# Optimization experiments

Hardware: AMD Instinct MI355X
Metric: run time of the kernel (lower is better)

## Reference

```python
import jax, jax.numpy as jnp
import numpy as np

B, C, H, W = 4, 128, 128, 128
NCLS = 80
NCONV = 2


def conv3x3(x, w, b):
    # x: [B,Cin,H,W], w: [Cout,Cin,3,3]
    y = jax.lax.conv_general_dilated(x, w, (1, 1), 'SAME',
                                     dimension_numbers=('NCHW', 'OIHW', 'NCHW'))
    return y + b[None, :, None, None]


def setup_inputs() -> dict:
    key = jax.random.key(0)
    ks = jax.random.split(key, 10)
    std = 0.01  # conv init std in the torch module
    prior_prob = 0.01
    bias_value = -np.log((1 - prior_prob) / prior_prob)
    inp = {
        'feature': jax.random.normal(ks[0], (B, C, H, W), jnp.float32),
        'targets': jax.random.uniform(ks[1], (B, NCLS, H, W), jnp.float32),
        'cls_w': std * jax.random.normal(ks[2], (NCONV, C, C, 3, 3), jnp.float32),
        'cls_b': jnp.zeros((NCONV, C), jnp.float32),
        'bbox_w': std * jax.random.normal(ks[3], (NCONV, C, C, 3, 3), jnp.float32),
        'bbox_b': jnp.zeros((NCONV, C), jnp.float32),
        'off_w': std * jax.random.normal(ks[4], (NCONV, C, C, 3, 3), jnp.float32),
        'off_b': jnp.zeros((NCONV, C), jnp.float32),
        'cls_score_w': std * jax.random.normal(ks[5], (NCLS, C, 3, 3), jnp.float32),
        'cls_score_b': jnp.full((NCLS,), bias_value, jnp.float32),
        'bbox_pred_w': std * jax.random.normal(ks[6], (2, C, 3, 3), jnp.float32),
        'bbox_pred_b': jnp.zeros((2,), jnp.float32),
        'center_off_w': std * jax.random.normal(ks[7], (2, C, 3, 3), jnp.float32),
        'center_off_b': jnp.zeros((2,), jnp.float32),
        'K': 100,
    }
    return inp


def centernet_forward(feature, targets, cls_w, cls_b, bbox_w, bbox_b, off_w, off_b,
                      cls_score_w, cls_score_b, bbox_pred_w, bbox_pred_b,
                      center_off_w, center_off_b, K):
    # ---- head: three conv+ReLU subnets + final 3x3 heads ----
    xc, xb, xo = feature, feature, feature
    for i in range(NCONV):
        xc = jax.nn.relu(conv3x3(xc, cls_w[i], cls_b[i]))
        xb = jax.nn.relu(conv3x3(xb, bbox_w[i], bbox_b[i]))
        xo = jax.nn.relu(conv3x3(xo, off_w[i], off_b[i]))
    logits = conv3x3(xc, cls_score_w, cls_score_b)      # [B,NCLS,H,W]
    wh = conv3x3(xb, bbox_pred_w, bbox_pred_b)          # [B,2,H,W]
    off = conv3x3(xo, center_off_w, center_off_b)       # [B,2,H,W]

    # ---- center focal loss (alpha=2, beta=4, reduction='sum') ----
    pos = (targets == 1.0).astype(logits.dtype)
    neg = (targets < 1.0).astype(logits.dtype)
    neg_w = jnp.power(1.0 - targets, 4.0)
    p = jax.nn.sigmoid(logits)
    log_p = jax.nn.log_sigmoid(logits)        # log(sigmoid(x))
    log_1mp = jax.nn.log_sigmoid(-logits)     # log(1 - sigmoid(x))
    pos_loss = log_p * jnp.square(1.0 - p) * pos
    neg_loss = log_1mp * jnp.square(p) * neg_w * neg
    loss = -(pos_loss.sum()) - (neg_loss.sum())

    # ---- decode: sigmoid + 3x3 maxpool pseudo-NMS + top-k + gather ----
    hm = p  # sigmoid heatmap
    hmax = jax.lax.reduce_window(hm, -jnp.inf, jax.lax.max,
                                 (1, 1, 3, 3), (1, 1, 1, 1), 'SAME')
    hm_nms = jnp.where(hmax == hm, hm, 0.0)
    scores, inds = jax.lax.top_k(hm_nms.reshape(B, -1), K)  # [B,K]
    hw = H * W
    clses = inds // hw                 # [B,K] int class ids
    sp = inds % hw                     # spatial index
    ys = (sp // W).astype(jnp.float32)
    xs = (sp % W).astype(jnp.float32)
    # gather wh/offset at peak locations
    wh_k = jnp.take_along_axis(wh.reshape(B, 2, hw), sp[:, None, :], axis=2)    # [B,2,K]
    off_k = jnp.take_along_axis(off.reshape(B, 2, hw), sp[:, None, :], axis=2)  # [B,2,K]
    cx = xs + off_k[:, 0]
    cy = ys + off_k[:, 1]
    w_, h_ = wh_k[:, 0], wh_k[:, 1]
    boxes = jnp.stack([cx - w_ / 2, cy - h_ / 2, cx + w_ / 2, cy + h_ / 2], axis=-1)  # [B,K,4]
    return boxes, scores, clses, loss


def reference(feature, targets, cls_w, cls_b, bbox_w, bbox_b, off_w, off_b,
              cls_score_w, cls_score_b, bbox_pred_w, bbox_pred_b,
              center_off_w, center_off_b, K):
    return centernet_forward(feature, targets, cls_w, cls_b, bbox_w, bbox_b,
                             off_w, off_b, cls_score_w, cls_score_b,
                             bbox_pred_w, bbox_pred_b, center_off_w,
                             center_off_b, K)
```

## Files before the change

kernel.cpp:

```cpp
#include <hip/hip_runtime.h>
#include <hip/hip_bf16.h>
#include <math.h>

#define B_    4
#define C_    128
#define H_    128
#define W_    128
#define HW_   (H_*W_)
#define NCLS_ 80
#define KTOP  100
#define CAPB  2048

typedef __attribute__((ext_vector_type(8)))  short bf16x8;
typedef __attribute__((ext_vector_type(16))) float f32x16;

#define WSTG_B     16384
#define WIMG_B     589824
#define NIMG       7
#define XROWB      144
#define XCOLS      130
#define XPITCH     (XCOLS * XROWB)
#define XSZ        ((size_t)16 * 130 * XPITCH)
#define XLDS_B     25920
#define LDS_TOT    (2 * XLDS_B)
#define ZERO_N     20512

__device__ __forceinline__ unsigned bf16_rne(float x) {
    unsigned u = __float_as_uint(x);
    return (u + 0x7FFFu + ((u >> 16) & 1u)) >> 16;
}
__device__ __forceinline__ void split2(float v0, float v1, unsigned& hiP, unsigned& loP) {
    unsigned h0 = bf16_rne(v0), h1 = bf16_rne(v1);
    float r0 = v0 - __uint_as_float(h0 << 16);
    float r1 = v1 - __uint_as_float(h1 << 16);
    unsigned l0 = bf16_rne(r0), l1 = bf16_rne(r1);
    hiP = h0 | (h1 << 16);
    loP = l0 | (l1 << 16);
}

#define MFMA32(a, bvec, c) __builtin_amdgcn_mfma_f32_32x32x16_bf16(a, bvec, c, 0, 0, 0)

__global__ __launch_bounds__(256) void init_k(char* __restrict__ xbase, int nbuf,
                                              unsigned* __restrict__ sm, float* __restrict__ loss)
{
    const int i = blockIdx.x * 256 + threadIdx.x;
    const int nb = nbuf * 8256;
    if (i < nb) {
        char* buf = xbase + (size_t)(i / 8256) * XSZ;
        const int j = i % 8256;
        int R, col;
        if (j < 4160) {
            const int g = j / 260, rr = j % 260;
            R = g * 130 + ((rr < 130) ? 0 : 129);
            col = rr % 130;
        } else {
            const int q = j - 4160;
            const int g = q / 256, m = q % 256;
            R = g * 130 + 1 + (m >> 1);
            col = (m & 1) ? 129 : 0;
        }
        char* p = buf + ((size_t)R * XCOLS + col) * XROWB;
        #pragma unroll
        for (int k = 0; k < 9; k++) *(uint4*)(p + k * 16) = make_uint4(0, 0, 0, 0);
    } else {
        const int k = i - nb;
        if (k < ZERO_N) sm[k] = 0u;
        if (k == ZERO_N) *loss = 0.f;
    }
}

struct WtArgs { const float* src[NIMG]; int cout[NIMG]; };

__global__ __launch_bounds__(256) void wtx_k(WtArgs a, unsigned short* wt)
{
    const int img = blockIdx.z;
    const int idx = blockIdx.x * 256 + threadIdx.x;
    const int h  = idx & 1;
    const int ks = (idx >> 1) & 1;
    const int r  = (idx >> 2) & 31;
    const int g  = (idx >> 7) & 3;
    const int st = idx >> 9;
    if (st >= 36) return;
    const int tap = st % 9, chunk = st / 9;
    const float* w = a.src[img];
    const int Cout = a.cout[img];
    const int cout = g * 32 + r;
    const int cin0 = chunk * 32 + ks * 16 + h * 8;
    float v[8];
    #pragma unroll
    for (int j = 0; j < 8; j++)
        v[j] = (cout < Cout) ? w[((size_t)cout * 128 + cin0 + j) * 9 + tap] : 0.f;
    unsigned hiW[4], loW[4];
    #pragma unroll
    for (int j = 0; j < 4; j++) split2(v[2 * j], v[2 * j + 1], hiW[j], loW[j]);
    char* dst = (char*)wt + (size_t)img * WIMG_B + (size_t)st * WSTG_B
              + g * 4096 + ks * 2048 + r * 32 + h * 16;
    *(uint4*)dst          = make_uint4(hiW[0], hiW[1], hiW[2], hiW[3]);
    *(uint4*)(dst + 1024) = make_uint4(loW[0], loW[1], loW[2], loW[3]);
}

template<int RELU, int XOUT>
__device__ __forceinline__ void conv_epilogue(
    f32x16 (&acc)[2][2], const bool* act,
    const float* bias, float* outf, char* outx, int Cout,
    int b, int x0, int y0, int wm, int wn, int kh, int l31)
{
    #pragma unroll
    for (int f = 0; f < 2; f++) {
        if (!act[f]) continue;
        if (XOUT == 0) {
            #pragma unroll
            for (int r = 0; r < 16; r++) {
                const int co = wm * 64 + f * 32 + 4 * kh + (r & 3) + 8 * (r >> 2);
                if (co < Cout) {
                    const float bv = bias[co];
                    #pragma unroll
                    for (int fn = 0; fn < 2; fn++) {
                        const int p = wn * 64 + fn * 32 + l31;
                        float v = acc[f][fn][r] + bv;
                        if (RELU) v = fmaxf(v, 0.f);
                        outf[((size_t)b * Cout + co) * HW_ + (size_t)(y0 + (p >> 4)) * 128 + (x0 + (p & 15))] = v;
                    }
                }
// ... 106 lines not shown
            if ((unsigned)gy < 128u && (unsigned)gx < 128u) {                 \
                const float* p0 = inb + (size_t)((ch) * 32 + 2 * cp) * HW_    \
                                      + gy * 128 + gx;                        \
                v0 = p0[0]; v1 = p0[HW_];                                     \
            }                                                                 \
        }                                                                     \
        xa[it] = v0; xb[it] = v1;                                             \
    }                                                                         \
} while (0)

#define STOREX_F(bufsel) do {                                                 \
    _Pragma("unroll")                                                         \
    for (int it = 0; it < 12; it++) {                                         \
        const int idx = t + it * 256;                                         \
        const int pl = idx & 15, cp = (idx >> 4) & 15, ph = idx >> 8;         \
        const int pos = ph * 16 + pl;                                         \
        if (pos < 180) {                                                      \
            unsigned hiP, loP; split2(xa[it], xb[it], hiP, loP);              \
            *(unsigned*)(lds + (bufsel) * XLDS_B + pos * 144 + 4 * cp)      = hiP; \
            *(unsigned*)(lds + (bufsel) * XLDS_B + pos * 144 + 64 + 4 * cp) = loP; \
        }                                                                     \
    }                                                                         \
} while (0)

#define TAPF_(CH, TAP, CUR, NXT) do {                                         \
    if ((CH) * 9 + (TAP) + 1 < 36) WLOAD_(NXT, (CH) * 9 + (TAP) + 1);         \
    MFMA_TAP_(CUR, (((TAP) / 3) * 18 + ((TAP) % 3)) * 144 + ((CH) & 1) * XLDS_B); \
} while (0)

#define CHUNKF_(CH, SA, SB) do {                                              \
    TAPF_(CH, 0, SA, SB); TAPF_(CH, 1, SB, SA); TAPF_(CH, 2, SA, SB);         \
    TAPF_(CH, 3, SB, SA); TAPF_(CH, 4, SA, SB); TAPF_(CH, 5, SB, SA);         \
    if ((CH) < 3) LOADX_F((CH) + 1);                                          \
    TAPF_(CH, 6, SA, SB); TAPF_(CH, 7, SB, SA); TAPF_(CH, 8, SA, SB);         \
    if ((CH) < 3) { STOREX_F(((CH) + 1) & 1); __syncthreads(); }              \
} while (0)

#define CONVF_MAIN()                                                          \
    bf16x8 wf[2][8];                                                          \
    WLOAD_(0, 0);                                                             \
    float xa[12], xb[12];                                                     \
    LOADX_F(0);                                                               \
    STOREX_F(0);                                                              \
    __syncthreads();                                                          \
    CHUNKF_(0, 0, 1);                                                         \
    CHUNKF_(1, 1, 0);                                                         \
    CHUNKF_(2, 0, 1);                                                         \
    CHUNKF_(3, 1, 0);

template<int RELU, int XOUT>
__global__ __launch_bounds__(256, 2) void conv_f_k(
    const float* __restrict__ in, const unsigned short* __restrict__ wt,
    const float* __restrict__ bias, float* __restrict__ outf,
    char* __restrict__ outx, int Cout)
{
    CONVF_SETUP();
    bool act[2];
    #pragma unroll
    for (int f = 0; f < 2; f++) act[f] = (wm * 64 + f * 32) < Cout;
    const char* wb = (const char*)wt + wm * 8192 + wlane;
    const float* inb = in + (size_t)b * 128 * HW_;
    CONVF_MAIN();
    conv_epilogue<RELU, XOUT>(acc, act, bias, outf, outx, Cout, b, x0, y0, wm, wn, kh, l31);
}

struct F3Args { const unsigned short* wt[3]; const float* bias[3]; char* outx[3]; };

__global__ __launch_bounds__(256, 2) void convF3_k(const float* __restrict__ in, F3Args a)
{
    const int ty = blockIdx.y;
    const unsigned short* wt = a.wt[ty];
    const float* bias = a.bias[ty];
    char* outx = a.outx[ty];

    CONVF_SETUP();
    bool act[2]; act[0] = true; act[1] = true;
    const char* wb = (const char*)wt + wm * 8192 + wlane;
    const float* inb = in + (size_t)b * 128 * HW_;
    CONVF_MAIN();
    conv_epilogue<1, 1>(acc, act, bias, nullptr, outx, 128, b, x0, y0, wm, wn, kh, l31);
}

#define CONVX_SETUP()                                                         \
    __shared__ __align__(16) char lds[LDS_TOT];                               \
    const int t    = threadIdx.x;                                             \
    const int lane = t & 63;                                                  \
    const int wv   = t >> 6;                                                  \
    const int wm   = wv >> 1;                                                 \
    const int wn   = wv & 1;                                                  \
    const int l31  = lane & 31;                                               \
    const int kh   = lane >> 5;                                               \
    const int bi = blockIdx.x;                                                \
    const int x0 = (bi & 7) << 4;                                             \
    const int y0 = ((bi >> 3) & 15) << 3;                                     \
    const int b  = bi >> 7;                                                   \
    int baddr[2];                                                             \
    _Pragma("unroll")                                                         \
    for (int fn = 0; fn < 2; fn++) {                                          \
        const int p = wn * 64 + fn * 32 + l31;                                \
        baddr[fn] = (p >> 4) * 2592 + (p & 15) * 144 + kh * 16;               \
    }                                                                         \
    const int wlane = ((lane & 31) << 5) | (kh << 4);                         \
    f32x16 acc[2][2];                                                         \
    _Pragma("unroll")                                                         \
    for (int i_ = 0; i_ < 2; i_++)                                            \
        _Pragma("unroll")                                                     \
        for (int j_ = 0; j_ < 2; j_++)                                        \
            _Pragma("unroll")                                                 \
            for (int r_ = 0; r_ < 16; r_++) acc[i_][j_][r_] = 0.f;

#define CONVX_PROLOG()                                                        \
    {                                                                         \
        const size_t rowbase = ((size_t)((b * 4 + 0) * 130 + y0) * XCOLS + x0) * XROWB; \
        _Pragma("unroll")                                                     \
        for (int gg = 0; gg < 5; gg++) {                                      \
            const int g = wv * 5 + gg;                                        \
            const int hy = g >> 1, i = g & 1;                                 \
            __builtin_amdgcn_global_load_lds(                                 \
                (const __attribute__((address_space(1))) unsigned*)           \
                    (xin + rowbase + (size_t)hy * XPITCH + i * 1024 + lane * 16), \
                (__attribute__((address_space(3))) unsigned*)(lds + hy * 2592 + i * 1024), \
                16, 0, 0);                                                    \
        }                                                                     \
        for (int u = t; u < 340; u += 256) {                                  \
            const int hy = u / 34;                                            \
            const int off = 2048 + (u % 34) * 16;                             \
            uint4 v = *(const uint4*)(xin + rowbase + (size_t)hy * XPITCH + off); \
            *(uint4*)(lds + hy * 2592 + off) = v;                             \
        }                                                                     \
    }                                                                         \
    __syncthreads();

#define TAPX_(CH, TAP, CUR, NXT) do {                                         \
    if ((CH) * 9 + (TAP) + 1 < 36) WLOAD_(NXT, (CH) * 9 + (TAP) + 1);         \
    MFMA_TAP_(CUR, ((TAP) / 3) * 2592 + ((TAP) % 3) * 144 + ((CH) & 1) * XLDS_B); \
} while (0)

#define CHUNKX_(CH, SA, SB) do {                                              \
    uint4 tl0_, tl1_; bool h1_ = false;                                       \
    const int xd_ = (((CH) + 1) & 1) * XLDS_B;                                \
    if ((CH) < 3) {                                                           \
        const size_t rowb1_ = ((size_t)((b * 4 + (CH) + 1) * 130 + y0) * XCOLS + x0) * XROWB; \
        _Pragma("unroll")                                                     \
        for (int gg = 0; gg < 5; gg++) {                                      \
            const int g = wv * 5 + gg;                                        \
            const int hy = g >> 1, ii = g & 1;                                \
            __builtin_amdgcn_global_load_lds(                                 \
                (const __attribute__((address_space(1))) unsigned*)           \
                    (xin + rowb1_ + (size_t)hy * XPITCH + ii * 1024 + lane * 16), \
                (__attribute__((address_space(3))) unsigned*)(lds + xd_ + hy * 2592 + ii * 1024), \
                16, 0, 0);                                                    \
        }                                                                     \
        {                                                                     \
            const int hy = t / 34, off = 2048 + (t % 34) * 16;                \
            tl0_ = *(const uint4*)(xin + rowb1_ + (size_t)hy * XPITCH + off); \
        }                                                                     \
        h1_ = (t < 84);                                                       \
        if (h1_) {                                                            \
            const int u = t + 256;                                            \
            const int hy = u / 34, off = 2048 + (u % 34) * 16;                \
            tl1_ = *(const uint4*)(xin + rowb1_ + (size_t)hy * XPITCH + off); \
        }                                                                     \
    }                                                                         \
    TAPX_(CH, 0, SA, SB); TAPX_(CH, 1, SB, SA); TAPX_(CH, 2, SA, SB);         \
    TAPX_(CH, 3, SB, SA); TAPX_(CH, 4, SA, SB); TAPX_(CH, 5, SB, SA);         \
    TAPX_(CH, 6, SA, SB); TAPX_(CH, 7, SB, SA); TAPX_(CH, 8, SA, SB);         \
    if ((CH) < 3) {                                                           \
        {                                                                     \
            const int hy = t / 34, off = 2048 + (t % 34) * 16;                \
            *(uint4*)(lds + xd_ + hy * 2592 + off) = tl0_;                    \
        }                                                                     \
        if (h1_) {                                                            \
            const int u = t + 256;                                            \
            const int hy = u / 34, off = 2048 + (u % 34) * 16;                \
            *(uint4*)(lds + xd_ + hy * 2592 + off) = tl1_;                    \
        }                                                                     \
        __syncthreads();                                                      \
    }                                                                         \
} while (0)

#define CONVX_MAIN()                                                          \
    bf16x8 wf[2][8];                                                          \
    WLOAD_(0, 0);                                                             \
    CONVX_PROLOG();                                                           \
    CHUNKX_(0, 0, 1);                                                         \
    CHUNKX_(1, 1, 0);                                                         \
    CHUNKX_(2, 0, 1);                                                         \
    CHUNKX_(3, 1, 0);

template<int RELU, int XOUT>
__global__ __launch_bounds__(256, 2) void conv_x_k(
    const char* __restrict__ xin, const unsigned short* __restrict__ wt,
    const float* __restrict__ bias, float* __restrict__ outf,
    char* __restrict__ outx, int Cout)
{
    CONVX_SETUP();
    bool act[2];
    #pragma unroll
    for (int f = 0; f < 2; f++) act[f] = (wm * 64 + f * 32) < Cout;
    const char* wb = (const char*)wt + wm * 8192 + wlane;
    CONVX_MAIN();
    conv_epilogue<RELU, XOUT>(acc, act, bias, outf, outx, Cout, b, x0, y0, wm, wn, kh, l31);
}

struct X3Args {
    const char* xin[3]; const unsigned short* wt[3]; const float* bias[3];
    float* outf[3]; char* outx[3]; int xout[3];
};

__global__ __launch_bounds__(256, 2) void convX3_k(X3Args a)
{
    const int ty = blockIdx.y;
    const char* xin = a.xin[ty];
    const unsigned short* wt = a.wt[ty];
    const float* bias = a.bias[ty];
    float* outf = a.outf[ty];
    char* outx = a.outx[ty];
    const int xo = a.xout[ty];

    CONVX_SETUP();
    bool act[2]; act[0] = true; act[1] = true;
    const char* wb = (const char*)wt + wm * 8192 + wlane;
    CONVX_MAIN();
    if (xo) conv_epilogue<1, 1>(acc, act, bias, nullptr, outx, 128, b, x0, y0, wm, wn, kh, l31);
    else    conv_epilogue<1, 0>(acc, act, bias, outf, nullptr, 128, b, x0, y0, wm, wn, kh, l31);
}

__device__ __forceinline__ void conv2out_body(
    const float* in, const float* w, const float* bias, float* out)
{
    __shared__ float ws[128 * 9 * 2];
    const int t = threadIdx.x;
    for (int i = t; i < 2304; i += 256) {
        const int co = i & 1, tap = (i >> 1) % 9, ci = i / 18;
        ws[i] = w[(size_t)co * 1152 + ci * 9 + tap];
    }
    __syncthreads();

    const int b  = blockIdx.y;
    const int y  = (blockIdx.x >> 3) * 16 + (t >> 4);
    const int x  = (blockIdx.x & 7) * 16 + (t & 15);
    const float* inb = in + (size_t)b * 128 * HW_ + y * 128 + x;

    float a0 = bias[0], a1 = bias[1];
    #pragma unroll 2
    for (int ci = 0; ci < 128; ci++) {
        const float* p  = inb + (size_t)ci * HW_;
        const float* wp = ws + ci * 18;
        #pragma unroll
        for (int tap = 0; tap < 9; tap++) {
            const int dy = tap / 3 - 1, dx = tap % 3 - 1;
            const int yy = y + dy, xx = x + dx;
            float v = 0.f;
            if ((unsigned)yy < 128u && (unsigned)xx < 128u) v = p[dy * 128 + dx];
            a0 = fmaf(v, wp[tap * 2 + 0], a0);
            a1 = fmaf(v, wp[tap * 2 + 1], a1);
        }
    }
    out[((size_t)b * 2 + 0) * HW_ + y * 128 + x] = a0;
    out[((size_t)b * 2 + 1) * HW_ + y * 128 + x] = a1;
}

__global__ __launch_bounds__(256) void conv2out_k(
    const float* __restrict__ in, const float* __restrict__ w,
    const float* __restrict__ bias, float* __restrict__ out)
{
    conv2out_body(in, w, bias, out);
}

__global__ __launch_bounds__(256) void conv2out2_k(
    const float* in0, const float* in1,
    const float* w0, const float* w1,
    const float* b0, const float* b1,
    float* out0, float* out1)
{
    const int z = blockIdx.z;
    conv2out_body(z ? in1 : in0, z ? w1 : w0, z ? b1 : b0, z ? out1 : out0);
}

__global__ __launch_bounds__(256) void lnh_k(
    const float* __restrict__ L, const float* __restrict__ targets,
    float* __restrict__ loss_out, unsigned* __restrict__ keys,
    unsigned* __restrict__ hist)
{
    __shared__ unsigned h[2048];
    for (int j = threadIdx.x; j < 2048; j += 256) h[j] = 0;
    __syncthreads();

    const int per_b = NCLS_ * HW_;
    const int b = blockIdx.y;
    const float* Lb = L + (size_t)b * per_b;
    const float* Tb = targets + (size_t)b * per_b;
    unsigned* kb = keys + (size_t)b * per_b;

    float sum = 0.f;
    for (int i = blockIdx.x * 256 + threadIdx.x; i < per_b; i += gridDim.x * 256) {
        const float x = Lb[i];
        const float t = Tb[i];
        const float e   = expf(-fabsf(x));
        const float inv = 1.f / (1.f + e);
        const float lp  = log1pf(e);
        const bool  xe  = (x >= 0.f);
        const float p   = xe ? inv : e * inv;
        const float lsp = xe ? -lp : (x - lp);
        const float lsn = lsp - x;
        float om = 1.f - t;
        float nw = om * om; nw *= nw;
        const float omp = 1.f - p;
        if (t == 1.0f)     sum -= lsp * omp * omp;
        else if (t < 1.0f) sum -= lsn * p * p * nw;

        const int sp = i & (HW_ - 1);
        const int y = sp >> 7, xq = sp & 127;
        const float* plane = Lb + (i - sp);
        const int ym = (y > 0) ? y - 1 : 0,   yp = (y < 127) ? y + 1 : 127;
        const int xm = (xq > 0) ? xq - 1 : 0, xp = (xq < 127) ? xq + 1 : 127;
        const float* r0 = plane + ym * 128;
        const float* r1 = plane + y  * 128;
        const float* r2 = plane + yp * 128;
        float m = fmaxf(fmaxf(fmaxf(r0[xm], r0[xq]), fmaxf(r0[xp], r1[xm])),
                 fmaxf(fmaxf(x, r1[xp]),
                 fmaxf(fmaxf(r2[xm], r2[xq]), r2[xp])));
        const float em   = expf(-fabsf(m));
        const float invm = 1.f / (1.f + em);
        const float pm   = (m >= 0.f) ? invm : em * invm;
        const unsigned key = (__float_as_uint(p) == __float_as_uint(pm)) ? __float_as_uint(p) : 0u;
        kb[i] = key;
        if (key) atomicAdd(&h[key >> 21], 1u);
    }

    #pragma unroll
    for (int off = 32; off > 0; off >>= 1) sum += __shfl_down(sum, off, 64);
    __shared__ float wsum[4];
    int lane = threadIdx.x & 63, wid = threadIdx.x >> 6;
    if (lane == 0) wsum[wid] = sum;
    __syncthreads();
    if (threadIdx.x == 0)
        atomicAdd(loss_out, wsum[0] + wsum[1] + wsum[2] + wsum[3]);

    unsigned* gh = hist + b * 2048;
    for (int j = threadIdx.x; j < 2048; j += 256) if (h[j]) atomicAdd(&gh[j], h[j]);
}

__global__ void hist2_k(const unsigned* __restrict__ keys, const unsigned* __restrict__ bin1,
                        unsigned* __restrict__ hist)
{
    __shared__ unsigned h[2048];
    for (int j = threadIdx.x; j < 2048; j += blockDim.x) h[j] = 0;
    __syncthreads();
    const int per_b = NCLS_ * HW_;
    const int b = blockIdx.y;
    const unsigned b1 = bin1[b];
    const unsigned* kb = keys + (size_t)b * per_b;
    for (int i = blockIdx.x * blockDim.x + threadIdx.x; i < per_b; i += gridDim.x * blockDim.x) {
        unsigned k = kb[i];
        if (k && (k >> 21) == b1) atomicAdd(&h[(k >> 10) & 2047], 1u);
    }
    __syncthreads();
    unsigned* gh = hist + b * 2048;
    for (int j = threadIdx.x; j < 2048; j += blockDim.x) if (h[j]) atomicAdd(&gh[j], h[j]);
}

__global__ void hist3_k(const unsigned* __restrict__ keys, const unsigned* __restrict__ pfx2,
                        unsigned* __restrict__ hist)
{
    __shared__ unsigned h[1024];
    for (int j = threadIdx.x; j < 1024; j += blockDim.x) h[j] = 0;
    __syncthreads();
    const int per_b = NCLS_ * HW_;
    const int b = blockIdx.y;
    const unsigned p2 = pfx2[b];
    const unsigned* kb = keys + (size_t)b * per_b;
    for (int i = blockIdx.x * blockDim.x + threadIdx.x; i < per_b; i += gridDim.x * blockDim.x) {
        unsigned k = kb[i];
        if (k && (k >> 10) == p2) atomicAdd(&h[k & 1023], 1u);
    }
    __syncthreads();
    unsigned* gh = hist + b * 1024;
    for (int j = threadIdx.x; j < 1024; j += blockDim.x) if (h[j]) atomicAdd(&gh[j], h[j]);
}

template<int NBINS, int LEVEL>
__global__ __launch_bounds__(256) void scan_k(
    const unsigned* __restrict__ hist,
    const unsigned* __restrict__ inPfx, const unsigned* __restrict__ inGt,
    unsigned* __restrict__ outPfx, unsigned* __restrict__ outGt)
{
    constexpr int PER = NBINS / 256;
    const int b = blockIdx.x;
    const int t = threadIdx.x;
    const unsigned* h = hist + b * NBINS;
    const unsigned base = (LEVEL == 1) ? 0u : inGt[b];

    unsigned v[PER];
    unsigned local = 0;
    #pragma unroll
    for (int i = 0; i < PER; i++) { v[i] = h[t * PER + i]; local += v[i]; }

    __shared__ unsigned ps[256];
    ps[t] = local;
    __syncthreads();
    #pragma unroll
    for (int off = 1; off < 256; off <<= 1) {
        unsigned add = (t + off < 256) ? ps[t + off] : 0u;
        __syncthreads();
        ps[t] += add;
        __syncthreads();
    }
    const unsigned sumAbove = (t == 255) ? 0u : ps[t + 1];

    unsigned sfx = sumAbove;
    #pragma unroll
    for (int i = PER - 1; i >= 0; i--) {
        unsigned sfx_next = sfx;
        sfx += v[i];
        bool cond     = (base + sfx      >= KTOP);
        bool condNext = (base + sfx_next >= KTOP);
        if (cond && !condNext) {
            unsigned sel = (unsigned)(t * PER + i);
            unsigned pfx = (LEVEL == 1) ? sel
                         : (LEVEL == 2) ? ((inPfx[b] << 11) | sel)
                                        : ((inPfx[b] << 10) | sel);
            outPfx[b] = pfx;
            outGt[b]  = base + sfx_next;
        }
    }
    if (t == 0 && base + ps[0] < KTOP) {
        unsigned pfx = (LEVEL == 1) ? 0u
                     : (LEVEL == 2) ? (inPfx[b] << 11)
                                    : (inPfx[b] << 10);
        outPfx[b] = pfx;
        outGt[b]  = base + ps[0];
    }
}

__global__ void select_k(const unsigned* __restrict__ keys, const unsigned* __restrict__ Tk,
                         unsigned* cntA, unsigned* cntB,
                         uint2* __restrict__ listA, unsigned* __restrict__ listB)
{
    const int per_b = NCLS_ * HW_;
    const int b = blockIdx.y;
    const unsigned T = Tk[b];
    const unsigned* kb = keys + (size_t)b * per_b;
    for (int i = blockIdx.x * blockDim.x + threadIdx.x; i < per_b; i += gridDim.x * blockDim.x) {
        unsigned k = kb[i];
        if (k > T) {
            unsigned pos = atomicAdd(&cntA[b], 1u);
            if (pos < KTOP) listA[b * KTOP + pos] = make_uint2(k, (unsigned)i);
        } else if (k == T && k != 0u) {
            unsigned pos = atomicAdd(&cntB[b], 1u);
            if (pos < CAPB) listB[b * CAPB + pos] = (unsigned)i;
        }
    }
}

__global__ void finalize_k(const unsigned* __restrict__ cntA, const unsigned* __restrict__ cntB,
                           const uint2* __restrict__ listA, const unsigned* __restrict__ listB,
                           const unsigned* __restrict__ Tk,
                           const float* __restrict__ wh, const float* __restrict__ off,
                           float* __restrict__ out)
{
    __shared__ unsigned sk[KTOP], si[KTOP], ok[KTOP], oi[KTOP];
    const int b = blockIdx.x;
    const int nA = (int)min(cntA[b], (unsigned)KTOP);
    const unsigned T = Tk[b];

    if ((int)threadIdx.x < nA) {
        uint2 e = listA[b * KTOP + threadIdx.x];
        sk[threadIdx.x] = e.x;
        si[threadIdx.x] = e.y;
    }
    __syncthreads();

    if (threadIdx.x == 0) {
        int need = KTOP - nA;
        unsigned nB = min(cntB[b], (unsigned)CAPB);
        long long prev = -1;
        for (int r = 0; r < need; r++) {
            unsigned best = 0xFFFFFFFFu;
            for (unsigned j = 0; j < nB; j++) {
                unsigned idx = listB[b * CAPB + j];
                if ((long long)idx > prev && idx < best) best = idx;
            }
            if (best == 0xFFFFFFFFu) { sk[nA + r] = 0u; si[nA + r] = 0u; }
            else { sk[nA + r] = T; si[nA + r] = best; prev = (long long)best; }
        }
    }
    __syncthreads();

    if (threadIdx.x < KTOP) {
        unsigned kk = sk[threadIdx.x], ii = si[threadIdx.x];
        int rank = 0;
        for (int j = 0; j < KTOP; j++) {
            unsigned kj = sk[j], ij = si[j];
            rank += (kj > kk) || (kj == kk && ij < ii);
        }
        ok[rank] = kk; oi[rank] = ii;
    }
    __syncthreads();

    if (threadIdx.x < KTOP) {
        int r = threadIdx.x;
        unsigned ind = oi[r];
        float score = __uint_as_float(ok[r]);
        int cls = (int)(ind / HW_);
        int sp  = (int)(ind % HW_);
        float ysf = (float)(sp >> 7);
        float xsf = (float)(sp & 127);
        float w0 = wh[((size_t)b * 2 + 0) * HW_ + sp];
        float h0 = wh[((size_t)b * 2 + 1) * HW_ + sp];
        float o0 = off[((size_t)b * 2 + 0) * HW_ + sp];
        float o1 = off[((size_t)b * 2 + 1) * HW_ + sp];
        float cx = xsf + o0;
        float cy = ysf + o1;
        float* boxes  = out;
        float* scores = out + (size_t)B_ * KTOP * 4;
        float* clses  = out + (size_t)B_ * KTOP * 5;
        boxes[((size_t)b * KTOP + r) * 4 + 0] = cx - w0 * 0.5f;
        boxes[((size_t)b * KTOP + r) * 4 + 1] = cy - h0 * 0.5f;
        boxes[((size_t)b * KTOP + r) * 4 + 2] = cx + w0 * 0.5f;
        boxes[((size_t)b * KTOP + r) * 4 + 3] = cy + h0 * 0.5f;
        scores[b * KTOP + r] = score;
        clses[b * KTOP + r]  = (float)cls;
    }
}

extern "C" void kernel_launch(void* const* d_in, const int* in_sizes, int n_in,
                              void* d_out, int out_size, void* d_ws, size_t ws_size,
                              hipStream_t stream)
{
    const float* feature      = (const float*)d_in[0];
    const float* targets      = (const float*)d_in[1];
    const float* cls_w        = (const float*)d_in[2];
    const float* cls_b        = (const float*)d_in[3];
    const float* bbox_w       = (const float*)d_in[4];
    const float* bbox_b       = (const float*)d_in[5];
    const float* off_w        = (const float*)d_in[6];
    const float* off_b        = (const float*)d_in[7];
    const float* cls_score_w  = (const float*)d_in[8];
    const float* cls_score_b  = (const float*)d_in[9];
    const float* bbox_pred_w  = (const float*)d_in[10];
    const float* bbox_pred_b  = (const float*)d_in[11];
    const float* center_off_w = (const float*)d_in[12];
    const float* center_off_b = (const float*)d_in[13];
    float* out = (float*)d_out;

    const size_t L_BYTES  = (size_t)B_ * NCLS_ * HW_ * 4;
    const size_t P_BYTES  = (size_t)B_ * 2 * HW_ * 4;
    const size_t WT_BYTES = (size_t)NIMG * WIMG_B;
    const size_t SM_BYTES = (size_t)1 << 18;

    char* ws = (char*)d_ws;
    const size_t lw = (size_t)C_ * C_ * 9;
    float* loss_ptr = out + (size_t)B_ * KTOP * 6;

    WtArgs wa;
    wa.src[0] = cls_w;        wa.cout[0] = 128;
    wa.src[1] = bbox_w;       wa.cout[1] = 128;
    wa.src[2] = off_w;        wa.cout[2] = 128;
    wa.src[3] = cls_w + lw;   wa.cout[3] = 128;
    wa.src[4] = bbox_w + lw;  wa.cout[4] = 128;
    wa.src[5] = off_w + lw;   wa.cout[5] = 128;
    wa.src[6] = cls_score_w;  wa.cout[6] = NCLS_;

    const size_t FUSED_NEED = 6 * XSZ + 2 * P_BYTES + WT_BYTES + SM_BYTES;

    #define WIMG(i) (WT + (size_t)(i) * (WIMG_B / 2))

    if (ws_size >= FUSED_NEED) {
        char* XA0 = ws;
        char* XA1 = ws + XSZ;
        char* XA2 = ws + 2 * XSZ;
        char* XB  = ws + 3 * XSZ;
        float* Bfb = (float*)(ws + 4 * XSZ);
        float* Bfo = (float*)(ws + 5 * XSZ);
        float* L   = (float*)XA0;
        unsigned* keys = (unsigned*)XA1;
        float* WH  = (float*)(ws + 6 * XSZ);
        float* OFF = (float*)(ws + 6 * XSZ + P_BYTES);
        unsigned short* WT = (unsigned short*)(ws + 6 * XSZ + 2 * P_BYTES);
        unsigned* sm = (unsigned*)(ws + 6 * XSZ + 2 * P_BYTES + WT_BYTES);

        unsigned* hist1 = sm;
        unsigned* hist2 = sm + 4 * 2048;
        unsigned* hist3 = sm + 8 * 2048;
        unsigned* bin1  = sm + 8 * 2048 + 4 * 1024;
        unsigned* gt1   = bin1 + 4;
        unsigned* pfx2  = bin1 + 8;
        unsigned* gt2   = bin1 + 12;
        unsigned* Tk    = bin1 + 16;
        unsigned* gt3   = bin1 + 20;
        unsigned* cntA  = bin1 + 24;
        unsigned* cntB  = bin1 + 28;
        uint2*    listA = (uint2*)(bin1 + 32);
        unsigned* listB = (unsigned*)(bin1 + 32 + 2 * B_ * KTOP);

        init_k<<<210, 256, 0, stream>>>(XA0, 4, sm, loss_ptr);
        wtx_k<<<dim3(72, 1, NIMG), 256, 0, stream>>>(wa, WT);

        F3Args f3;
        f3.wt[0] = WIMG(0); f3.bias[0] = cls_b;  f3.outx[0] = XA0;
        f3.wt[1] = WIMG(1); f3.bias[1] = bbox_b; f3.outx[1] = XA1;
        f3.wt[2] = WIMG(2); f3.bias[2] = off_b;  f3.outx[2] = XA2;
        convF3_k<<<dim3(512, 3), 256, 0, stream>>>(feature, f3);

        X3Args x3;
        x3.xin[0] = XA0; x3.wt[0] = WIMG(3); x3.bias[0] = cls_b + C_;
        x3.outf[0] = nullptr; x3.outx[0] = XB; x3.xout[0] = 1;
        x3.xin[1] = XA1; x3.wt[1] = WIMG(4); x3.bias[1] = bbox_b + C_;
        x3.outf[1] = Bfb; x3.outx[1] = nullptr; x3.xout[1] = 0;
        x3.xin[2] = XA2; x3.wt[2] = WIMG(5); x3.bias[2] = off_b + C_;
        x3.outf[2] = Bfo; x3.outx[2] = nullptr; x3.xout[2] = 0;
        convX3_k<<<dim3(512, 3), 256, 0, stream>>>(x3);

        conv_x_k<0, 0><<<512, 256, 0, stream>>>(XB, WIMG(6), cls_score_b, L, nullptr, NCLS_);
        conv2out2_k<<<dim3(64, 4, 2), 256, 0, stream>>>(
            Bfb, Bfo, bbox_pred_w, center_off_w, bbox_pred_b, center_off_b, WH, OFF);

        lnh_k<<<dim3(512, B_), 256, 0, stream>>>(L, targets, loss_ptr, keys, hist1);

        dim3 hgrid(512, B_);
        scan_k<2048, 1><<<B_, 256, 0, stream>>>(hist1, nullptr, nullptr, bin1, gt1);
        hist2_k<<<hgrid, 256, 0, stream>>>(keys, bin1, hist2);
        scan_k<2048, 2><<<B_, 256, 0, stream>>>(hist2, bin1, gt1, pfx2, gt2);
        hist3_k<<<hgrid, 256, 0, stream>>>(keys, pfx2, hist3);
        scan_k<1024, 3><<<B_, 256, 0, stream>>>(hist3, pfx2, gt2, Tk, gt3);
        select_k<<<hgrid, 256, 0, stream>>>(keys, Tk, cntA, cntB, listA, listB);

        finalize_k<<<B_, 128, 0, stream>>>(cntA, cntB, listA, listB, Tk, WH, OFF, out);
    } else {
        char* XA = ws;
        char* XB = ws + XSZ;
        float* L   = (float*)(ws + 2 * XSZ);
        float* WH  = (float*)(ws + 2 * XSZ + L_BYTES);
        float* OFF = (float*)(ws + 2 * XSZ + L_BYTES + P_BYTES);
        unsigned short* WT = (unsigned short*)(ws + 2 * XSZ + L_BYTES + 2 * P_BYTES);
        unsigned* sm = (unsigned*)(ws + 2 * XSZ + L_BYTES + 2 * P_BYTES + WT_BYTES);
        float* Bf = (float*)XB;
        unsigned* keys = (unsigned*)XB;

        unsigned* hist1 = sm;
        unsigned* hist2 = sm + 4 * 2048;
        unsigned* hist3 = sm + 8 * 2048;
        unsigned* bin1  = sm + 8 * 2048 + 4 * 1024;
        unsigned* gt1   = bin1 + 4;
        unsigned* pfx2  = bin1 + 8;
        unsigned* gt2   = bin1 + 12;
        unsigned* Tk    = bin1 + 16;
        unsigned* gt3   = bin1 + 20;
        unsigned* cntA  = bin1 + 24;
        unsigned* cntB  = bin1 + 28;
        uint2*    listA = (uint2*)(bin1 + 32);
        unsigned* listB = (unsigned*)(bin1 + 32 + 2 * B_ * KTOP);

        init_k<<<145, 256, 0, stream>>>(XA, 2, sm, loss_ptr);
        wtx_k<<<dim3(72, 1, NIMG), 256, 0, stream>>>(wa, WT);

        conv_f_k<1, 1><<<512, 256, 0, stream>>>(feature, WIMG(0), cls_b,       nullptr, XA, 128);
        conv_x_k<1, 1><<<512, 256, 0, stream>>>(XA,      WIMG(3), cls_b + C_,  nullptr, XB, 128);
        conv_x_k<0, 0><<<512, 256, 0, stream>>>(XB,      WIMG(6), cls_score_b, L, nullptr, NCLS_);
        conv_f_k<1, 1><<<512, 256, 0, stream>>>(feature, WIMG(1), bbox_b,      nullptr, XA, 128);
        conv_x_k<1, 0><<<512, 256, 0, stream>>>(XA,      WIMG(4), bbox_b + C_, Bf, nullptr, 128);
        conv2out_k<<<dim3(64, 4), 256, 0, stream>>>(Bf, bbox_pred_w, bbox_pred_b, WH);
        conv_f_k<1, 1><<<512, 256, 0, stream>>>(feature, WIMG(2), off_b,       nullptr, XA, 128);
        conv_x_k<1, 0><<<512, 256, 0, stream>>>(XA,      WIMG(5), off_b + C_,  Bf, nullptr, 128);
        conv2out_k<<<dim3(64, 4), 256, 0, stream>>>(Bf, center_off_w, center_off_b, OFF);

        lnh_k<<<dim3(512, B_), 256, 0, stream>>>(L, targets, loss_ptr, keys, hist1);

        dim3 hgrid(512, B_);
        scan_k<2048, 1><<<B_, 256, 0, stream>>>(hist1, nullptr, nullptr, bin1, gt1);
        hist2_k<<<hgrid, 256, 0, stream>>>(keys, bin1, hist2);
        scan_k<2048, 2><<<B_, 256, 0, stream>>>(hist2, bin1, gt1, pfx2, gt2);
        hist3_k<<<hgrid, 256, 0, stream>>>(keys, pfx2, hist3);
        scan_k<1024, 3><<<B_, 256, 0, stream>>>(hist3, pfx2, gt2, Tk, gt3);
        select_k<<<hgrid, 256, 0, stream>>>(keys, Tk, cntA, cntB, listA, listB);

        finalize_k<<<B_, 128, 0, stream>>>(cntA, cntB, listA, listB, Tk, WH, OFF, out);
    }
}
```

Baseline: 548.1 us.

## Fold scan/finalize into last-block of histogram kernels and merge score conv with heads

The separate scan kernels and the finalize kernel are folded into the preceding histogram and select kernels using a last-block-done atomic counter, so the last block to finish runs the scan or finalize. The class-score conv and the two small 2-channel head convs are merged into a single launch with a blockIdx split. The aim is to cut kernel launches and inter-kernel gaps on the serial top-k chain. In exchange, the last block does serial work on a single CU, and the cross-block handoff depends on atomics and fences.

```diff
diff --git a/kernel.cpp b/kernel.cpp
--- a/kernel.cpp
+++ b/kernel.cpp
@@ -23,7 +23,7 @@
 #define XSZ        ((size_t)16 * 130 * XPITCH)
 #define XLDS_B     25920
 #define LDS_TOT    (2 * XLDS_B)
-#define ZERO_N     20512
+#define ZERO_N     20516
 
 __device__ __forceinline__ unsigned bf16_rne(float x) {
     unsigned u = __float_as_uint(x);
@@ -39,6 +39,15 @@
 }
 
 #define MFMA32(a, bvec, c) __builtin_amdgcn_mfma_f32_32x32x16_bf16(a, bvec, c, 0, 0, 0)
+
+__device__ __forceinline__ bool last_block(unsigned* done) {
+    __threadfence();
+    __syncthreads();
+    __shared__ unsigned lb_rank_;
+    if (threadIdx.x == 0) lb_rank_ = atomicAdd(done, 1u);
+    __syncthreads();
+    return lb_rank_ == gridDim.x * gridDim.y - 1;
+}
 
 __global__ __launch_bounds__(256) void init_k(char* __restrict__ xbase, int nbuf,
                                               unsigned* __restrict__ sm, float* __restrict__ loss)
@@ -311,7 +320,6 @@
 }
 
 #define CONVX_SETUP()                                                         \
-    __shared__ __align__(16) char lds[LDS_TOT];                               \
     const int t    = threadIdx.x;                                             \
     const int lane = t & 63;                                                  \
     const int wv   = t >> 6;                                                  \
@@ -423,6 +431,7 @@
     const float* __restrict__ bias, float* __restrict__ outf,
     char* __restrict__ outx, int Cout)
 {
+    __shared__ __align__(16) char lds[LDS_TOT];
     CONVX_SETUP();
     bool act[2];
     #pragma unroll
@@ -439,6 +448,7 @@
 
 __global__ __launch_bounds__(256, 2) void convX3_k(X3Args a)
 {
+    __shared__ __align__(16) char lds[LDS_TOT];
     const int ty = blockIdx.y;
     const char* xin = a.xin[ty];
     const unsigned short* wt = a.wt[ty];
@@ -456,9 +466,9 @@
 }
 
 __device__ __forceinline__ void conv2out_body(
-    const float* in, const float* w, const float* bias, float* out)
-{
-    __shared__ float ws[128 * 9 * 2];
+    const float* in, const float* w, const float* bias, float* out,
+    int gx, int b, float* ws)
+{
     const int t = threadIdx.x;
     for (int i = t; i < 2304; i += 256) {
         const int co = i & 1, tap = (i >> 1) % 9, ci = i / 18;
@@ -466,9 +476,8 @@
     }
     __syncthreads();
 
-    const int b  = blockIdx.y;
-    const int y  = (blockIdx.x >> 3) * 16 + (t >> 4);
-    const int x  = (blockIdx.x & 7) * 16 + (t & 15);
+    const int y  = (gx >> 3) * 16 + (t >> 4);
+    const int x  = (gx & 7) * 16 + (t & 15);
     const float* inb = in + (size_t)b * 128 * HW_ + y * 128 + x;
 
     float a0 = bias[0], a1 = bias[1];
@@ -494,23 +503,100 @@
     const float* __restrict__ in, const float* __restrict__ w,
     const float* __restrict__ bias, float* __restrict__ out)
 {
-    conv2out_body(in, w, bias, out);
-}
-
-__global__ __launch_bounds__(256) void conv2out2_k(
-    const float* in0, const float* in1,
-    const float* w0, const float* w1,
-    const float* b0, const float* b1,
-    float* out0, float* out1)
-{
-    const int z = blockIdx.z;
-    conv2out_body(z ? in1 : in0, z ? w1 : w0, z ? b1 : b0, z ? out1 : out0);
+    __shared__ float ws[2304];
+    conv2out_body(in, w, bias, out, blockIdx.x, blockIdx.y, ws);
+}
+
+__global__ __launch_bounds__(256, 2) void sc_k(
+    const char* __restrict__ xbin, const unsigned short* __restrict__ wt,
+    const float* __restrict__ sbias, float* __restrict__ Lout,
+    const float* __restrict__ inb0, const float* __restrict__ inb1,
+    const float* __restrict__ w0, const float* __restrict__ w1,
+    const float* __restrict__ hb0, const float* __restrict__ hb1,
+    float* __restrict__ WH, float* __restrict__ OFF)
+{
+    __shared__ __align__(16) char lds[LDS_TOT];
+    if (blockIdx.x < 512) {
+        const char* xin = xbin;
+        CONVX_SETUP();
+        bool act[2];
+        act[0] = true; act[1] = (64 < NCLS_);
+        const char* wb = (const char*)wt + wm * 8192 + wlane;
+        CONVX_MAIN();
+        conv_epilogue<0, 0>(acc, act, sbias, Lout, nullptr, NCLS_, b, x0, y0, wm, wn, kh, l31);
+    } else {
+        const int j = blockIdx.x - 512;
+        const int gx = j & 63, bb = (j >> 6) & 3, z = j >> 8;
+        conv2out_body(z ? inb1 : inb0, z ? w1 : w0, z ? hb1 : hb0, z ? OFF : WH,
+                      gx, bb, (float*)lds);
+    }
+}
+
+template<int NBINS, int LEVEL>
+__device__ __forceinline__ void scan_body(
+    unsigned* h, const unsigned* inPfx, const unsigned* inGt,
+    unsigned* outPfx, unsigned* outGt, int b)
+{
+    constexpr int PER = NBINS / 256;
+    const int t = threadIdx.x;
+    const unsigned base = (LEVEL == 1) ? 0u : inGt[b];
+
+    unsigned v[PER];
+    unsigned local = 0;
+    #pragma unroll
+    for (int i = 0; i < PER; i++) { v[i] = atomicAdd(&h[t * PER + i], 0u); local += v[i]; }
+
+    __shared__ unsigned ps[256];
+    ps[t] = local;
+    __syncthreads();
+    #pragma unroll
+    for (int off = 1; off < 256; off <<= 1) {
+        unsigned add = (t + off < 256) ? ps[t + off] : 0u;
+        __syncthreads();
+        ps[t] += add;
+        __syncthreads();
+    }
+    const unsigned sumAbove = (t == 255) ? 0u : ps[t + 1];
+
+    unsigned sfx = sumAbove;
+    #pragma unroll
+    for (int i = PER - 1; i >= 0; i--) {
+        unsigned sfx_next = sfx;
+        sfx += v[i];
+        bool cond     = (base + sfx      >= KTOP);
+        bool condNext = (base + sfx_next >= KTOP);
+        if (cond && !condNext) {
+            unsigned sel = (unsigned)(t * PER + i);
+            unsigned pfx = (LEVEL == 1) ? sel
+                         : (LEVEL == 2) ? ((inPfx[b] << 11) | sel)
+                                        : ((inPfx[b] << 10) | sel);
+            outPfx[b] = pfx;
+            outGt[b]  = base + sfx_next;
+        }
+    }
+    if (t == 0 && base + ps[0] < KTOP) {
+        unsigned pfx = (LEVEL == 1) ? 0u
+                     : (LEVEL == 2) ? (inPfx[b] << 11)
+                                    : (inPfx[b] << 10);
+        outPfx[b] = pfx;
+        outGt[b]  = base + ps[0];
+    }
+}
+
+template<int NBINS, int LEVEL>
+__global__ __launch_bounds__(256) void scan_k(
+    unsigned* __restrict__ hist,
+    const unsigned* __restrict__ inPfx, const unsigned* __restrict__ inGt,
+    unsigned* __restrict__ outPfx, unsigned* __restrict__ outGt)
+{
+    scan_body<NBINS, LEVEL>(hist + blockIdx.x * NBINS, inPfx, inGt, outPfx, outGt, blockIdx.x);
 }
 
 __global__ __launch_bounds__(256) void lnh_k(
     const float* __restrict__ L, const float* __restrict__ targets,
     float* __restrict__ loss_out, unsigned* __restrict__ keys,
-    unsigned* __restrict__ hist)
+    unsigned* __restrict__ hist,
+    unsigned* done, unsigned* outPfx, unsigned* outGt)
 {
     __shared__ unsigned h[2048];
     for (int j = threadIdx.x; j < 2048; j += 256) h[j] = 0;
@@ -569,10 +655,19 @@
 
     unsigned* gh = hist + b * 2048;
     for (int j = threadIdx.x; j < 2048; j += 256) if (h[j]) atomicAdd(&gh[j], h[j]);
-}
-
-__global__ void hist2_k(const unsigned* __restrict__ keys, const unsigned* __restrict__ bin1,
-                        unsigned* __restrict__ hist)
+
+    if (done && last_block(done)) {
+        for (int bb = 0; bb < B_; bb++) {
+            scan_body<2048, 1>(hist + bb * 2048, nullptr, nullptr, outPfx, outGt, bb);
+            __syncthreads();
+        }
+    }
+}
+
+__global__ __launch_bounds__(256) void hist2_k(
+    const unsigned* __restrict__ keys, const unsigned* __restrict__ bin1,
+    unsigned* __restrict__ hist,
+    unsigned* done, const unsigned* inGt, unsigned* outPfx, unsigned* outGt)
 {
     __shared__ unsigned h[2048];
     for (int j = threadIdx.x; j < 2048; j += blockDim.x) h[j] = 0;
@@ -588,10 +683,19 @@
     __syncthreads();
     unsigned* gh = hist + b * 2048;
     for (int j = threadIdx.x; j < 2048; j += blockDim.x) if (h[j]) atomicAdd(&gh[j], h[j]);
-}
-
-__global__ void hist3_k(const unsigned* __restrict__ keys, const unsigned* __restrict__ pfx2,
-                        unsigned* __restrict__ hist)
+
+    if (done && last_block(done)) {
+        for (int bb = 0; bb < B_; bb++) {
+            scan_body<2048, 2>(hist + bb * 2048, bin1, inGt, outPfx, outGt, bb);
+            __syncthreads();
+        }
+    }
+}
+
+__global__ __launch_bounds__(256) void hist3_k(
+    const unsigned* __restrict__ keys, const unsigned* __restrict__ pfx2,
+    unsigned* __restrict__ hist,
+    unsigned* done, const unsigned* inGt, unsigned* outPfx, unsigned* outGt)
 {
     __shared__ unsigned h[1024];
     for (int j = threadIdx.x; j < 1024; j += blockDim.x) h[j] = 0;
@@ -607,108 +711,42 @@
     __syncthreads();
     unsigned* gh = hist + b * 1024;
     for (int j = threadIdx.x; j < 1024; j += blockDim.x) if (h[j]) atomicAdd(&gh[j], h[j]);
-}
-
-template<int NBINS, int LEVEL>
-__global__ __launch_bounds__(256) void scan_k(
-    const unsigned* __restrict__ hist,
-    const unsigned* __restrict__ inPfx, const unsigned* __restrict__ inGt,
-    unsigned* __restrict__ outPfx, unsigned* __restrict__ outGt)
-{
-    constexpr int PER = NBINS / 256;
-    const int b = blockIdx.x;
+
+    if (done && last_block(done)) {
+        for (int bb = 0; bb < B_; bb++) {
+            scan_body<1024, 3>(hist + bb * 1024, pfx2, inGt, outPfx, outGt, bb);
+            __syncthreads();
+        }
+    }
+}
+
+__device__ __forceinline__ void finalize_body(
+    unsigned long long* listA, unsigned* listB,
+    const unsigned* Tk, unsigned* cntA, unsigned* cntB,
+    const float* wh, const float* off, float* out, int b)
+{
+    __shared__ unsigned sk[KTOP], si[KTOP], ok[KTOP], oi[KTOP];
+    __shared__ unsigned lbs[CAPB];
     const int t = threadIdx.x;
-    const unsigned* h = hist + b * NBINS;
-    const unsigned base = (LEVEL == 1) ? 0u : inGt[b];
-
-    unsigned v[PER];
-    unsigned local = 0;
-    #pragma unroll
-    for (int i = 0; i < PER; i++) { v[i] = h[t * PER + i]; local += v[i]; }
-
-    __shared__ unsigned ps[256];
-    ps[t] = local;
-    __syncthreads();
-    #pragma unroll
-    for (int off = 1; off < 256; off <<= 1) {
-        unsigned add = (t + off < 256) ? ps[t + off] : 0u;
-        __syncthreads();
-        ps[t] += add;
-        __syncthreads();
-    }
-    const unsigned sumAbove = (t == 255) ? 0u : ps[t + 1];
-
-    unsigned sfx = sumAbove;
-    #pragma unroll
-    for (int i = PER - 1; i >= 0; i--) {
-        unsigned sfx_next = sfx;
-        sfx += v[i];
-        bool cond     = (base + sfx      >= KTOP);
-        bool condNext = (base + sfx_next >= KTOP);
-        if (cond && !condNext) {
-            unsigned sel = (unsigned)(t * PER + i);
-            unsigned pfx = (LEVEL == 1) ? sel
-                         : (LEVEL == 2) ? ((inPfx[b] << 11) | sel)
-                                        : ((inPfx[b] << 10) | sel);
-            outPfx[b] = pfx;
-            outGt[b]  = base + sfx_next;
-        }
-    }
-    if (t == 0 && base + ps[0] < KTOP) {
-        unsigned pfx = (LEVEL == 1) ? 0u
-                     : (LEVEL == 2) ? (inPfx[b] << 11)
-                                    : (inPfx[b] << 10);
-        outPfx[b] = pfx;
-        outGt[b]  = base + ps[0];
-    }
-}
-
-__global__ void select_k(const unsigned* __restrict__ keys, const unsigned* __restrict__ Tk,
-                         unsigned* cntA, unsigned* cntB,
-                         uint2* __restrict__ listA, unsigned* __restrict__ listB)
-{
-    const int per_b = NCLS_ * HW_;
-    const int b = blockIdx.y;
+    const int nA = (int)min(atomicAdd(&cntA[b], 0u), (unsigned)KTOP);
+    const unsigned nB = min(atomicAdd(&cntB[b], 0u), (unsigned)CAPB);
     const unsigned T = Tk[b];
-    const unsigned* kb = keys + (size_t)b * per_b;
-    for (int i = blockIdx.x * blockDim.x + threadIdx.x; i < per_b; i += gridDim.x * blockDim.x) {
-        unsigned k = kb[i];
-        if (k > T) {
-            unsigned pos = atomicAdd(&cntA[b], 1u);
-            if (pos < KTOP) listA[b * KTOP + pos] = make_uint2(k, (unsigned)i);
-        } else if (k == T && k != 0u) {
-            unsigned pos = atomicAdd(&cntB[b], 1u);
-            if (pos < CAPB) listB[b * CAPB + pos] = (unsigned)i;
-        }
-    }
-}
-
-__global__ void finalize_k(const unsigned* __restrict__ cntA, const unsigned* __restrict__ cntB,
-                           const uint2* __restrict__ listA, const unsigned* __restrict__ listB,
-                           const unsigned* __restrict__ Tk,
-                           const float* __restrict__ wh, const float* __restrict__ off,
-                           float* __restrict__ out)
-{
-    __shared__ unsigned sk[KTOP], si[KTOP], ok[KTOP], oi[KTOP];
-    const int b = blockIdx.x;
-    const int nA = (int)min(cntA[b], (unsigned)KTOP);
-    const unsigned T = Tk[b];
-
-    if ((int)threadIdx.x < nA) {
-        uint2 e = listA[b * KTOP + threadIdx.x];
-        sk[threadIdx.x] = e.x;
-        si[threadIdx.x] = e.y;
-    }
-    __syncthreads();
-
-    if (threadIdx.x == 0) {
+
+    if (t < nA) {
+        unsigned long long v = atomicAdd(&listA[b * KTOP + t], 0ull);
+        sk[t] = (unsigned)v;
+        si[t] = (unsigned)(v >> 32);
+    }
+    for (int j = t; j < (int)nB; j += 256) lbs[j] = atomicAdd(&listB[b * CAPB + j], 0u);
+    __syncthreads();
+
+    if (t == 0) {
         int need = KTOP - nA;
-        unsigned nB = min(cntB[b], (unsigned)CAPB);
         long long prev = -1;
         for (int r = 0; r < need; r++) {
             unsigned best = 0xFFFFFFFFu;
             for (unsigned j = 0; j < nB; j++) {
-                unsigned idx = listB[b * CAPB + j];
+                unsigned idx = lbs[j];
                 if ((long long)idx > prev && idx < best) best = idx;
             }
             if (best == 0xFFFFFFFFu) { sk[nA + r] = 0u; si[nA + r] = 0u; }
@@ -717,8 +755,8 @@
     }
     __syncthreads();
 
-    if (threadIdx.x < KTOP) {
-        unsigned kk = sk[threadIdx.x], ii = si[threadIdx.x];
+    if (t < KTOP) {
+        unsigned kk = sk[t], ii = si[t];
         int rank = 0;
         for (int j = 0; j < KTOP; j++) {
             unsigned kj = sk[j], ij = si[j];
@@ -728,8 +766,8 @@
     }
     __syncthreads();
 
-    if (threadIdx.x < KTOP) {
-        int r = threadIdx.x;
+    if (t < KTOP) {
+        int r = t;
         unsigned ind = oi[r];
         float score = __uint_as_float(ok[r]);
         int cls = (int)(ind / HW_);
@@ -754,6 +792,48 @@
     }
 }
 
+__global__ __launch_bounds__(256) void finalize_k(
+    unsigned long long* listA, unsigned* listB,
+    const unsigned* __restrict__ Tk, unsigned* cntA, unsigned* cntB,
+    const float* __restrict__ wh, const float* __restrict__ off,
+    float* __restrict__ out)
+{
+    finalize_body(listA, listB, Tk, cntA, cntB, wh, off, out, blockIdx.x);
+}
+
+__global__ __launch_bounds__(256) void select_k(
+    const unsigned* __restrict__ keys, const unsigned* __restrict__ Tk,
+    unsigned* cntA, unsigned* cntB,
+    unsigned long long* __restrict__ listA, unsigned* __restrict__ listB,
+    unsigned* done,
+    const float* __restrict__ wh, const float* __restrict__ off,
+    float* __restrict__ out)
+{
+    const int per_b = NCLS_ * HW_;
+    const int b = blockIdx.y;
+    const unsigned T = Tk[b];
+    const unsigned* kb = keys + (size_t)b * per_b;
+    for (int i = blockIdx.x * blockDim.x + threadIdx.x; i < per_b; i += gridDim.x * blockDim.x) {
+        unsigned k = kb[i];
+        if (k > T) {
+            unsigned pos = atomicAdd(&cntA[b], 1u);
+            if (pos < KTOP)
+                atomicExch(&listA[b * KTOP + pos],
+                           ((unsigned long long)(unsigned)i << 32) | (unsigned long long)k);
+        } else if (k == T && k != 0u) {
+            unsigned pos = atomicAdd(&cntB[b], 1u);
+            if (pos < CAPB) atomicExch(&listB[b * CAPB + pos], (unsigned)i);
+        }
+    }
+
+    if (done && last_block(done)) {
+        for (int bb = 0; bb < B_; bb++) {
+            finalize_body(listA, listB, Tk, cntA, cntB, wh, off, out, bb);
+            __syncthreads();
+        }
+    }
+}
+
 extern "C" void kernel_launch(void* const* d_in, const int* in_sizes, int n_in,
                               void* d_out, int out_size, void* d_ws, size_t ws_size,
                               hipStream_t stream)
@@ -796,6 +876,26 @@
 
     #define WIMG(i) (WT + (size_t)(i) * (WIMG_B / 2))
 
+    #define SM_LAYOUT()                                                       \
+        unsigned* hist1 = sm;                                                 \
+        unsigned* hist2 = sm + 4 * 2048;                                      \
+        unsigned* hist3 = sm + 8 * 2048;                                      \
+        unsigned* bin1  = sm + 8 * 2048 + 4 * 1024;                           \
+        unsigned* gt1   = bin1 + 4;                                           \
+        unsigned* pfx2  = bin1 + 8;                                           \
+        unsigned* gt2   = bin1 + 12;                                          \
+        unsigned* Tk    = bin1 + 16;                                          \
+        unsigned* gt3   = bin1 + 20;                                          \
+        unsigned* cntA  = bin1 + 24;                                          \
+        unsigned* cntB  = bin1 + 28;                                          \
+        unsigned* doneL = bin1 + 32;                                          \
+        unsigned* done2 = bin1 + 33;                                          \
+        unsigned* done3 = bin1 + 34;                                          \
+        unsigned* doneS = bin1 + 35;                                          \
+        unsigned long long* listA = (unsigned long long*)(bin1 + 36);         \
+        unsigned* listB = (unsigned*)(listA + (size_t)B_ * KTOP);             \
+        (void)gt3; (void)doneL; (void)done2; (void)done3; (void)doneS;
+
     if (ws_size >= FUSED_NEED) {
         char* XA0 = ws;
         char* XA1 = ws + XSZ;
@@ -809,20 +909,7 @@
         float* OFF = (float*)(ws + 6 * XSZ + P_BYTES);
         unsigned short* WT = (unsigned short*)(ws + 6 * XSZ + 2 * P_BYTES);
         unsigned* sm = (unsigned*)(ws + 6 * XSZ + 2 * P_BYTES + WT_BYTES);
-
-        unsigned* hist1 = sm;
-        unsigned* hist2 = sm + 4 * 2048;
-        unsigned* hist3 = sm + 8 * 2048;
-        unsigned* bin1  = sm + 8 * 2048 + 4 * 1024;
-        unsigned* gt1   = bin1 + 4;
-        unsigned* pfx2  = bin1 + 8;
-        unsigned* gt2   = bin1 + 12;
-        unsigned* Tk    = bin1 + 16;
-        unsigned* gt3   = bin1 + 20;
-        unsigned* cntA  = bin1 + 24;
-        unsigned* cntB  = bin1 + 28;
-        uint2*    listA = (uint2*)(bin1 + 32);
-        unsigned* listB = (unsigned*)(bin1 + 32 + 2 * B_ * KTOP);
+        SM_LAYOUT();
 
         init_k<<<210, 256, 0, stream>>>(XA0, 4, sm, loss_ptr);
         wtx_k<<<dim3(72, 1, NIMG), 256, 0, stream>>>(wa, WT);
@@ -842,21 +929,17 @@
         x3.outf[2] = Bfo; x3.outx[2] = nullptr; x3.xout[2] = 0;
         convX3_k<<<dim3(512, 3), 256, 0, stream>>>(x3);
 
-        conv_x_k<0, 0><<<512, 256, 0, stream>>>(XB, WIMG(6), cls_score_b, L, nullptr, NCLS_);
-        conv2out2_k<<<dim3(64, 4, 2), 256, 0, stream>>>(
-            Bfb, Bfo, bbox_pred_w, center_off_w, bbox_pred_b, center_off_b, WH, OFF);
-
-        lnh_k<<<dim3(512, B_), 256, 0, stream>>>(L, targets, loss_ptr, keys, hist1);
+        sc_k<<<1024, 256, 0, stream>>>(XB, WIMG(6), cls_score_b, L,
+                                       Bfb, Bfo, bbox_pred_w, center_off_w,
+                                       bbox_pred_b, center_off_b, WH, OFF);
 
         dim3 hgrid(512, B_);
-        scan_k<2048, 1><<<B_, 256, 0, stream>>>(hist1, nullptr, nullptr, bin1, gt1);
-        hist2_k<<<hgrid, 256, 0, stream>>>(keys, bin1, hist2);
-        scan_k<2048, 2><<<B_, 256, 0, stream>>>(hist2, bin1, gt1, pfx2, gt2);
-        hist3_k<<<hgrid, 256, 0, stream>>>(keys, pfx2, hist3);
-        scan_k<1024, 3><<<B_, 256, 0, stream>>>(hist3, pfx2, gt2, Tk, gt3);
-        select_k<<<hgrid, 256, 0, stream>>>(keys, Tk, cntA, cntB, listA, listB);
-
-        finalize_k<<<B_, 128, 0, stream>>>(cntA, cntB, listA, listB, Tk, WH, OFF, out);
+        lnh_k<<<hgrid, 256, 0, stream>>>(L, targets, loss_ptr, keys, hist1,
+                                         doneL, bin1, gt1);
+        hist2_k<<<hgrid, 256, 0, stream>>>(keys, bin1, hist2, done2, gt1, pfx2, gt2);
+        hist3_k<<<hgrid, 256, 0, stream>>>(keys, pfx2, hist3, done3, gt2, Tk, gt3);
+        select_k<<<hgrid, 256, 0, stream>>>(keys, Tk, cntA, cntB, listA, listB,
+                                            doneS, WH, OFF, out);
     } else {
         char* XA = ws;
         char* XB = ws + XSZ;
@@ -867,20 +950,7 @@
         unsigned* sm = (unsigned*)(ws + 2 * XSZ + L_BYTES + 2 * P_BYTES + WT_BYTES);
         float* Bf = (float*)XB;
         unsigned* keys = (unsigned*)XB;
-
-        unsigned* hist1 = sm;
-        unsigned* hist2 = sm + 4 * 2048;
-        unsigned* hist3 = sm + 8 * 2048;
-        unsigned* bin1  = sm + 8 * 2048 + 4 * 1024;
-        unsigned* gt1   = bin1 + 4;
-        unsigned* pfx2  = bin1 + 8;
-        unsigned* gt2   = bin1 + 12;
-        unsigned* Tk    = bin1 + 16;
-        unsigned* gt3   = bin1 + 20;
-        unsigned* cntA  = bin1 + 24;
-        unsigned* cntB  = bin1 + 28;
-        uint2*    listA = (uint2*)(bin1 + 32);
-        unsigned* listB = (unsigned*)(bin1 + 32 + 2 * B_ * KTOP);
+        SM_LAYOUT();
 
         init_k<<<145, 256, 0, stream>>>(XA, 2, sm, loss_ptr);
         wtx_k<<<dim3(72, 1, NIMG), 256, 0, stream>>>(wa, WT);
@@ -895,16 +965,16 @@
         conv_x_k<1, 0><<<512, 256, 0, stream>>>(XA,      WIMG(5), off_b + C_,  Bf, nullptr, 128);
         conv2out_k<<<dim3(64, 4), 256, 0, stream>>>(Bf, center_off_w, center_off_b, OFF);
 
-        lnh_k<<<dim3(512, B_), 256, 0, stream>>>(L, targets, loss_ptr, keys, hist1);
-
         dim3 hgrid(512, B_);
+        lnh_k<<<hgrid, 256, 0, stream>>>(L, targets, loss_ptr, keys, hist1,
+                                         nullptr, nullptr, nullptr);
         scan_k<2048, 1><<<B_, 256, 0, stream>>>(hist1, nullptr, nullptr, bin1, gt1);
-        hist2_k<<<hgrid, 256, 0, stream>>>(keys, bin1, hist2);
+        hist2_k<<<hgrid, 256, 0, stream>>>(keys, bin1, hist2, nullptr, nullptr, nullptr, nullptr);
         scan_k<2048, 2><<<B_, 256, 0, stream>>>(hist2, bin1, gt1, pfx2, gt2);
-        hist3_k<<<hgrid, 256, 0, stream>>>(keys, pfx2, hist3);
+        hist3_k<<<hgrid, 256, 0, stream>>>(keys, pfx2, hist3, nullptr, nullptr, nullptr, nullptr);
         scan_k<1024, 3><<<B_, 256, 0, stream>>>(hist3, pfx2, gt2, Tk, gt3);
-        select_k<<<hgrid, 256, 0, stream>>>(keys, Tk, cntA, cntB, listA, listB);
-
-        finalize_k<<<B_, 128, 0, stream>>>(cntA, cntB, listA, listB, Tk, WH, OFF, out);
-    }
-}
+        select_k<<<hgrid, 256, 0, stream>>>(keys, Tk, cntA, cntB, listA, listB,
+                                            nullptr, WH, OFF, out);
+        finalize_k<<<B_, 256, 0, stream>>>(listA, listB, Tk, cntA, cntB, WH, OFF, out);
+    }
+}
```

After: 1.099 ms. 100% more time.
